# Performance work log

Measured on AMD Instinct MI355X. Metric: run time of the kernel, lower is better.

## Reference

```python
import jax, jax.numpy as jnp
import numpy as np

EPS = 1e-5
DIL = 1
PAD = 1
STRIDE = 1

def conv2d(x, w, stride=1, pad=1, dil=1):
    return jax.lax.conv_general_dilated(x, w, (stride, stride), [(pad, pad), (pad, pad)],
                                        rhs_dilation=(dil, dil),
                                        dimension_numbers=('NCHW', 'OIHW', 'NCHW'))

def batchnorm(x, g, b, m, v):
    inv = g / jnp.sqrt(v + EPS)
    return x * inv[None, :, None, None] + (b - m * inv)[None, :, None, None]

def _bilinear(img, y, x):
    # img: [C,H,W]; y,x: [Ho,Wo] float sample coords; zero padding outside.
    H, W = img.shape[1], img.shape[2]
    y0 = jnp.floor(y); x0 = jnp.floor(x)
    ty = y - y0; tx = x - x0
    y0i = y0.astype(jnp.int32); x0i = x0.astype(jnp.int32)
    def g(yi, xi):
        valid = (yi >= 0) & (yi < H) & (xi >= 0) & (xi < W)
        v = img[:, jnp.clip(yi, 0, H - 1), jnp.clip(xi, 0, W - 1)]  # [C,Ho,Wo]
        return jnp.where(valid[None], v, jnp.zeros((), img.dtype))
    return (g(y0i, x0i) * ((1 - ty) * (1 - tx))[None]
            + g(y0i, x0i + 1) * ((1 - ty) * tx)[None]
            + g(y0i + 1, x0i) * (ty * (1 - tx))[None]
            + g(y0i + 1, x0i + 1) * (ty * tx)[None])

def deform_conv(x, w, offset, stride=1, pad=1, dil=1):
    # offset: [B, 18, Ho, Wo], channels 0:9 = dy per kernel tap (row-major), 9:18 = dx.
    B, C, H, W = x.shape
    Co = w.shape[0]
    Ho = (H + 2 * pad - dil * 2 - 1) // stride + 1
    Wo = (W + 2 * pad - dil * 2 - 1) // stride + 1
    off = offset.reshape(B, 2, 9, Ho, Wo)
    iy = (jnp.arange(Ho) * stride - pad).astype(x.dtype)
    ix = (jnp.arange(Wo) * stride - pad).astype(x.dtype)
    wk = w.reshape(Co, C, 9)
    out = jnp.zeros((B, Co, Ho, Wo), x.dtype)
    for k in range(9):  # fixed 3x3 kernel taps
        ky, kx = k // 3, k % 3
        ys = iy[:, None] + ky * dil + off[:, 0, k]  # [B,Ho,Wo]
        xs = ix[None, :] + kx * dil + off[:, 1, k]
        val = jax.vmap(_bilinear)(x, ys, xs)        # [B,C,Ho,Wo]
        out = out + jnp.einsum('bchw,oc->bohw', val, wk[:, :, k])
    return out

def offset_bias(dil, dtype):
    bw = jnp.array([[-1., 0., 1.]] * 3, dtype) * (dil - 1)
    bh = bw.T
    return jnp.concatenate([bh.reshape(-1), bw.reshape(-1)])  # [18]

def setup_inputs() -> dict:
    key = jax.random.key(0)
    ks = jax.random.split(key, 12)
    B, C, H, W = 8, 256, 56, 56
    inp = {
        'x': jax.random.normal(ks[0], (B, C, H, W), jnp.float32),
        'conv1_w': jax.random.normal(ks[1], (C, C, 3, 3), jnp.float32) * 0.02,
        'bn1_g': jax.random.normal(ks[2], (C,), jnp.float32) * 0.1 + 1.0,
        'bn1_b': jax.random.normal(ks[3], (C,), jnp.float32) * 0.1,
        'bn1_m': jax.random.normal(ks[4], (C,), jnp.float32) * 0.1,
        'bn1_v': jax.random.uniform(ks[5], (C,), jnp.float32) + 0.5,
        'off_w': jax.random.normal(ks[6], (18, C, 3, 3), jnp.float32) * 0.01,
        'off_b': jnp.zeros((18,), jnp.float32),
        'conv2_w': jax.random.normal(ks[7], (C, C, 3, 3), jnp.float32) * 0.02,
        'bn2_g': jax.random.normal(ks[8], (C,), jnp.float32) * 0.1 + 1.0,
        'bn2_b': jax.random.normal(ks[9], (C,), jnp.float32) * 0.1,
        'bn2_m': jax.random.normal(ks[10], (C,), jnp.float32) * 0.1,
        'bn2_v': jax.random.uniform(ks[11], (C,), jnp.float32) + 0.5,
    }
    return inp

def reference(x, conv1_w, bn1_g, bn1_b, bn1_m, bn1_v, off_w, off_b, conv2_w, bn2_g, bn2_b, bn2_m, bn2_v):
    residual = x
    out = conv2d(x, conv1_w, STRIDE, PAD, DIL)
    out = jax.nn.relu(batchnorm(out, bn1_g, bn1_b, bn1_m, bn1_v))
    offset = conv2d(out, off_w, STRIDE, PAD, DIL) + off_b[None, :, None, None]
    offset = offset + offset_bias(DIL, out.dtype)[None, :, None, None]
    out = deform_conv(out, conv2_w, offset, STRIDE, PAD, DIL)
    out = batchnorm(out, bn2_g, bn2_b, bn2_m, bn2_v)
    return jax.nn.relu(out + residual)
```

## Files before the change

kernel.cpp:

```cpp
#include <hip/hip_runtime.h>
#include <hip/hip_fp16.h>

#define NB 8
#define NH 56
#define NW 56
#define NHW 3136
#define NCHW 802816
#define NPIX 25088
#define NHP 58
#define EPSV 1e-5f
#define BUFS 20480
#define TOFN 451584

typedef float f32x4 __attribute__((ext_vector_type(4)));
typedef __bf16 bf16x8 __attribute__((ext_vector_type(8)));
typedef _Float16 f16x8 __attribute__((ext_vector_type(8)));

__device__ __forceinline__ unsigned short f2b(float f) {
  unsigned int u = __float_as_uint(f);
  u += 0x7FFFu + ((u >> 16) & 1u);
  return (unsigned short)(u >> 16);
}
__device__ __forceinline__ unsigned short f2h(float f) {
  return __half_as_ushort(__float2half(f));
}
__device__ __forceinline__ void soft_barrier() {
  __builtin_amdgcn_s_waitcnt(0xC07F);
  __builtin_amdgcn_s_barrier();
}
__device__ __forceinline__ void dma16(const unsigned short* g, unsigned short* l) {
  __builtin_amdgcn_global_load_lds(
      (const __attribute__((address_space(1))) unsigned int*)g,
      (__attribute__((address_space(3))) unsigned int*)l,
      16, 0, 0);
}
__device__ __forceinline__ unsigned int bil2(
    unsigned int c00, unsigned int c01, unsigned int c10, unsigned int c11,
    __half2 W00, __half2 W01, __half2 W10, __half2 W11) {
  __half2 v = __hmul2(W00, *(__half2*)&c00);
  v = __hfma2(W01, *(__half2*)&c01, v);
  v = __hfma2(W10, *(__half2*)&c10, v);
  v = __hfma2(W11, *(__half2*)&c11, v);
  return *(unsigned int*)&v;
}

__global__ __launch_bounds__(256) void clear_borders(
    unsigned short* __restrict__ xbp, unsigned short* __restrict__ t1b,
    float* __restrict__ tof)
{
  int i = blockIdx.x*256 + threadIdx.x;
  int q = i & 31; int pid = i >> 5;
  int b = pid / 228, j = pid % 228;
  int y, x;
  if (j < 58)       { y = 0;  x = j; }
  else if (j < 116) { y = 57; x = j - 58; }
  else { int jj = j - 116; y = 1 + (jj >> 1); x = (jj & 1) * 57; }
  size_t addr = ((size_t)(b*NHP + y)*NHP + x)*256 + q*8;
  uint4 z = make_uint4(0u,0u,0u,0u);
  *(uint4*)(xbp + addr) = z;
  *(uint4*)(t1b + addr) = z;
  int zi = i*8;
  if (zi < TOFN) {
    *(float4*)(tof + zi)     = make_float4(0.f,0.f,0.f,0.f);
    *(float4*)(tof + zi + 4) = make_float4(0.f,0.f,0.f,0.f);
  }
}

__global__ __launch_bounds__(256) void prep_x(
    const float* __restrict__ x, unsigned short* __restrict__ xbp)
{
  __shared__ float T[64][65];
  const int pxt  = blockIdx.x * 64;
  const int cg   = blockIdx.y * 64;
  const int b    = pxt / NHW;
  const int rem0 = pxt % NHW;
  const int t    = threadIdx.x;
  const int pl   = t & 63;
  const int c0   = t >> 6;
  const float* src = x + (size_t)b*NCHW + rem0;
  #pragma unroll
  for (int it = 0; it < 16; ++it) {
    int c = c0 + it*4;
    T[c][pl] = src[(size_t)(cg + c)*NHW + pl];
  }
  __syncthreads();
  const int pr = t >> 5;
  const int cp = t & 31;
  #pragma unroll
  for (int it = 0; it < 8; ++it) {
    int pxl = pr + it*8;
    int rem = rem0 + pxl;
    int ho = rem / NW, wo = rem % NW;
    unsigned int pk = ((unsigned int)f2b(T[cp*2+1][pxl]) << 16) | (unsigned int)f2b(T[cp*2][pxl]);
    *(unsigned int*)(xbp + ((size_t)(b*NHP + ho + 1)*NHP + (wo + 1))*256 + cg + cp*2) = pk;
  }
}

__global__ __launch_bounds__(256) void prep_w_all(
    const float* __restrict__ w1, const float* __restrict__ w2,
    const float* __restrict__ ow,
    unsigned short* __restrict__ w1p, unsigned short* __restrict__ w2p,
    unsigned short* __restrict__ w3p)
{
  int i = blockIdx.x*256 + threadIdx.x;
  if (i < 589824) {
    int co = i / 2304, r = i % 2304, k = r >> 8, ci = r & 255;
    w1p[i] = f2b(w1[((size_t)co*256 + ci)*9 + k]);
  } else if (i < 1179648) {
    int j = i - 589824;
    int co = j / 2304, r = j % 2304, k = r >> 8, ci = r & 255;
    w2p[j] = f2h(w2[((size_t)co*256 + ci)*9 + k]);
  } else {
    int j = i - 1179648;
    int co = j / 2304, r = j % 2304, k = r >> 8, ci = r & 255;
    w3p[j] = (co < 18) ? f2h(ow[((size_t)co*256 + ci)*9 + k]) : (unsigned short)0;
  }
}

__global__ __launch_bounds__(512, 4) void gemm_conv1(
    const unsigned short* __restrict__ xbp, const unsigned short* __restrict__ w1p,
    const float* __restrict__ gam, const float* __restrict__ bet,
    const float* __restrict__ mu,  const float* __restrict__ var,
    unsigned short* __restrict__ t1b)
{
  __shared__ unsigned short SMEM[2*BUFS];

  const int bx   = blockIdx.x;
  const int nbx  = (bx & 7)*49 + (bx >> 3);
  const int m0   = nbx * 64;
  const int t    = threadIdx.x;
  const int lane = t & 63;
  const int wv   = t >> 6;
  const int wvM  = wv & 1;
  const int wvN  = wv >> 1;
  const int quad = lane >> 4;
  const int l15  = lane & 15;

  const int srow = t >> 3;
  const int seg  = t & 7;
  const int swz8 = ((seg ^ (srow & 7))*8);
  const int px  = m0 + srow;
  const int b   = px / NHW, rem = px % NHW;
  const int ho  = rem / NW, wo = rem % NW;
  const unsigned int pbaseA = ((unsigned int)(b*NHP + ho)*NHP + wo)*256u + (unsigned int)swz8;
  const int rowB0 = wv*32 + (lane >> 3);
  const unsigned int bswz = (unsigned int)(((lane & 7) ^ (lane >> 3))*8);
  const int chA = wv*512;

  f32x4 acc[2][4];
  #pragma unroll
  for (int i = 0; i < 2; ++i)
    #pragma unroll
    for (int j = 0; j < 4; ++j) acc[i][j] = (f32x4)(0.f);

  {
    dma16(xbp + pbaseA, &SMEM[chA]);
    #pragma unroll
    for (int j = 0; j < 4; ++j)
      dma16(w1p + (size_t)(rowB0 + j*8)*2304 + bswz, &SMEM[4096 + (wv*4 + j)*512]);
    __syncthreads();
  }

  for (int r = 0; r < 36; ++r) {
    unsigned short* Ac = SMEM + (r & 1)*BUFS;
    unsigned short* Bc = Ac + 4096;
    unsigned short* An = SMEM + ((r + 1) & 1)*BUFS;
    unsigned short* Bn = An + 4096;
    {
      const int rn = (r < 35) ? r + 1 : 35;
      const int kn = rn >> 2, cicn = rn & 3;
      const int kyn = kn/3, kxn = kn - kyn*3;
      const unsigned int koff = (unsigned int)((kyn*NHP + kxn)*256 + cicn*64);
      dma16(xbp + pbaseA + koff, &An[chA]);
      const unsigned int rb = (unsigned int)(rn*64);
      #pragma unroll
      for (int j = 0; j < 4; ++j)
        dma16(w1p + (size_t)(rowB0 + j*8)*2304 + rb + bswz, &Bn[(wv*4 + j)*512]);
    }
    #pragma unroll
    for (int kk = 0; kk < 2; ++kk) {
      const int s8 = (kk*4 + quad) ^ (l15 & 7);
      bf16x8 af[2], bfr[4];
      #pragma unroll
      for (int mt = 0; mt < 2; ++mt)
        af[mt] = *(const bf16x8*)(&Ac[(wvM*32 + mt*16 + l15)*64 + s8*8]);
      #pragma unroll
      for (int nt = 0; nt < 4; ++nt)
        bfr[nt] = *(const bf16x8*)(&Bc[(wvN*64 + nt*16 + l15)*64 + s8*8]);
      #pragma unroll
      for (int mt = 0; mt < 2; ++mt)
        #pragma unroll
        for (int nt = 0; nt < 4; ++nt)
          acc[mt][nt] = __builtin_amdgcn_mfma_f32_16x16x32_bf16(af[mt], bfr[nt], acc[mt][nt], 0, 0, 0);
    }
    __syncthreads();
  }

  unsigned short* Sw = SMEM + wv*2304;
  #pragma unroll
  for (int nt = 0; nt < 4; ++nt) {
    const int co = wvN*64 + nt*16 + l15;
    const float inv  = gam[co] * rsqrtf(var[co] + EPSV);
    const float beta = bet[co] - mu[co]*inv;
    #pragma unroll
    for (int mt = 0; mt < 2; ++mt) {
      #pragma unroll
      for (int rr = 0; rr < 4; ++rr) {
        const int pxl = mt*16 + quad*4 + rr;
        float val = acc[mt][nt][rr]*inv + beta;
        val = val > 0.f ? val : 0.f;
        Sw[pxl*72 + nt*16 + l15] = f2h(val);
      }
    }
  }
  #pragma unroll
  for (int i = 0; i < 4; ++i) {
    const int pxl = (lane >> 3) + 8*i;
    const int sc  = lane & 7;
    uint4 q = *(const uint4*)(&Sw[pxl*72 + sc*8]);
    const int pg = m0 + wvM*32 + pxl;
    const int bb = pg / NHW, rm = pg % NHW;
    const int hh = rm / NW, ww = rm % NW;
    *(uint4*)(t1b + ((size_t)(bb*NHP + hh + 1)*NHP + ww + 1)*256 + wvN*64 + sc*8) = q;
  }
}

__global__ __launch_bounds__(256, 8) void gemm_off(
    const unsigned short* __restrict__ t1b, const unsigned short* __restrict__ w3p,
    const float* __restrict__ ob, float* __restrict__ toff)
{
  __shared__ unsigned short Al[4096];
  __shared__ unsigned short Bl[2048];

  const int bx  = blockIdx.x;
  const int nbx = (bx & 7)*49 + (bx >> 3);
  const int m0  = nbx * 64;
  const int kc = blockIdx.y;
  const int t    = threadIdx.x;
  const int lane = t & 63;
  const int wv   = t >> 6;
  const int quad = lane >> 4;
  const int l15  = lane & 15;

  const int arow = t >> 2;
  const int as4  = t & 3;
  const int axor = arow & 7;
  const int pxa  = m0 + arow;
  const int ba   = pxa / NHW, rema = pxa % NHW;
  const unsigned int pbase = ((unsigned int)(ba*NHP + rema/NW)*NHP + rema%NW)*256u;

  const int brow = t >> 3;
  const int bs   = t & 7;

  f32x4 acc[2];
  #pragma unroll
  for (int nt = 0; nt < 2; ++nt) {
    float init = 0.f;
    if (kc == 0) { int co = nt*16 + l15; init = (co < 18) ? ob[co] : 0.f; }
    acc[nt] = (f32x4)(init);
  }

  uint4 pA0, pA1, pB;
  {
    const int r = kc*9, k = r >> 2, cic = r & 3;
    const int ky = k/3, kx = k - ky*3;
    const unsigned int base = pbase + (unsigned int)((ky*NHP + kx)*256 + cic*64);
    pA0 = *(const uint4*)(t1b + base + as4*8);
    pA1 = *(const uint4*)(t1b + base + (as4+4)*8);
    pB  = *(const uint4*)(w3p + (size_t)brow*2304 + r*64 + bs*8);
  }

  for (int rr = 0; rr < 9; ++rr) {
    const int r = kc*9 + rr;
    __syncthreads();
    *(uint4*)(&Al[arow*64 + ((as4     ^ axor)*8)]) = pA0;
    *(uint4*)(&Al[arow*64 + (((as4+4) ^ axor)*8)]) = pA1;
    *(uint4*)(&Bl[brow*64 + ((bs ^ (brow & 7))*8)]) = pB;
    {
      const int rn = (rr < 8) ? r + 1 : r;
      const int kn = rn >> 2, cicn = rn & 3;
      const int kyn = kn/3, kxn = kn - kyn*3;
      const unsigned int base = pbase + (unsigned int)((kyn*NHP + kxn)*256 + cicn*64);
      pA0 = *(const uint4*)(t1b + base + as4*8);
      pA1 = *(const uint4*)(t1b + base + (as4+4)*8);
      pB  = *(const uint4*)(w3p + (size_t)brow*2304 + rn*64 + bs*8);
    }
    soft_barrier();
    #pragma unroll
    for (int kk = 0; kk < 2; ++kk) {
      const int s8 = (kk*4 + quad) ^ (l15 & 7);
      f16x8 af = *(const f16x8*)(&Al[(wv*16 + l15)*64 + s8*8]);
      #pragma unroll
      for (int nt = 0; nt < 2; ++nt) {
        f16x8 bfr = *(const f16x8*)(&Bl[(nt*16 + l15)*64 + s8*8]);
        acc[nt] = __builtin_amdgcn_mfma_f32_16x16x32_f16(af, bfr, acc[nt], 0, 0, 0);
      }
    }
  }
  #pragma unroll
  for (int nt = 0; nt < 2; ++nt) {
    const int co = nt*16 + l15;
    if (co < 18) {
      #pragma unroll
      for (int rr2 = 0; rr2 < 4; ++rr2) {
        const int pg = m0 + wv*16 + quad*4 + rr2;
        const int bb = pg / NHW, rm = pg % NHW;
        atomicAdd(&toff[(size_t)bb*(18*NHW) + (size_t)co*NHW + rm], acc[nt][rr2]);
      }
    }
  }
}

__global__ __launch_bounds__(512, 4) void gemm_deform(
    const unsigned short* __restrict__ t1b, const unsigned short* __restrict__ w2p,
    const float* __restrict__ toff, const float* __restrict__ xres,
    const float* __restrict__ gam, const float* __restrict__ bet,
    const float* __restrict__ mu,  const float* __restrict__ var,
    float* __restrict__ outp)
{
  __shared__ unsigned short SMEM[2*BUFS];

  const int bid  = blockIdx.x;
  const int nb   = (bid & 7)*49 + (bid >> 3);
  const int m0   = nb * 64;
  const int t    = threadIdx.x;
  const int lane = t & 63;
  const int wv   = t >> 6;
  const int wvM  = wv & 1;
  const int wvN  = wv >> 1;
  const int quad = lane >> 4;
  const int l15  = lane & 15;

  const int srow = t >> 3;
  const int seg  = t & 7;
  const int sxor = srow & 7;
  const int px   = m0 + srow;
  const int b    = px / NHW, rem = px % NHW;
  const int ho   = rem / NW, wo = rem % NW;
  const int obb  = b*(18*NHW) + rem;
  const unsigned int prowb = (unsigned int)(b*NHP);

  const int rowB0 = wv*32 + (lane >> 3);
  const unsigned int bswz = (unsigned int)(((lane & 7) ^ (lane >> 3))*8);

  f32x4 acc[2][4];
  #pragma unroll
  for (int i = 0; i < 2; ++i)
    #pragma unroll
    for (int j = 0; j < 4; ++j) acc[i][j] = (f32x4)(0.f);

  unsigned int o00, o01, o10, o11;
  __half2 W00, W01, W10, W11;
#define COORDS(KK) {                                                   \
    const int ky_ = (KK)/3, kx_ = (KK) - ky_*3;                        \
    const float offy = toff[obb + (KK)*NHW];                           \
    const float offx = toff[obb + (9+(KK))*NHW];                       \
    const float yf = (float)(ho - 1 + ky_) + offy;                     \
    const float xf = (float)(wo - 1 + kx_) + offx;                     \
    const float y0f = floorf(yf), x0f = floorf(xf);                    \
    const float ty = yf - y0f,   tx = xf - x0f;                        \
    const int y0p = (int)y0f + 1, x0p = (int)x0f + 1;                  \
    const int cy0 = min(max(y0p,   0), NHP-1);                         \
    const int cy1 = min(max(y0p+1, 0), NHP-1);                         \
    const int cx0 = min(max(x0p,   0), NHP-1);                         \
    const int cx1 = min(max(x0p+1, 0), NHP-1);                         \
    W00 = __float2half2_rn((1.f-ty)*(1.f-tx));                         \
    W01 = __float2half2_rn((1.f-ty)*tx);                               \
    W10 = __float2half2_rn(ty*(1.f-tx));                               \
    W11 = __float2half2_rn(ty*tx);                                     \
    o00 = ((prowb + cy0)*NHP + cx0)*256u + seg*8u;                     \
    o01 = ((prowb + cy0)*NHP + cx1)*256u + seg*8u;                     \
    o10 = ((prowb + cy1)*NHP + cx0)*256u + seg*8u;                     \
    o11 = ((prowb + cy1)*NHP + cx1)*256u + seg*8u;                     \
  }

#define PACKW(DST) {                                                            \
    uint4 res;                                                                  \
    res.x = bil2(pc00.x, pc01.x, pc10.x, pc11.x, W00, W01, W10, W11);           \
    res.y = bil2(pc00.y, pc01.y, pc10.y, pc11.y, W00, W01, W10, W11);           \
    res.z = bil2(pc00.z, pc01.z, pc10.z, pc11.z, W00, W01, W10, W11);           \
    res.w = bil2(pc00.w, pc01.w, pc10.w, pc11.w, W00, W01, W10, W11);           \
    *(uint4*)(&(DST)[srow*64 + ((seg ^ sxor)*8)]) = res;                        \
  }

#define ISSUEC(RN) {                                                           \
    const unsigned int cio_ = (unsigned int)(((RN) & 3)*64);                   \
    pc00 = *(const uint4*)(t1b + o00 + cio_);                                  \
    pc01 = *(const uint4*)(t1b + o01 + cio_);                                  \
    pc10 = *(const uint4*)(t1b + o10 + cio_);                                  \
    pc11 = *(const uint4*)(t1b + o11 + cio_);                                  \
  }

  uint4 pc00, pc01, pc10, pc11;

  COORDS(0);
  {
    ISSUEC(0);
    #pragma unroll
    for (int j = 0; j < 4; ++j)
      dma16(w2p + (size_t)(rowB0 + j*8)*2304 + bswz, &SMEM[4096 + (wv*4 + j)*512]);
    PACKW(SMEM);
    ISSUEC(1);
    __syncthreads();
  }

  for (int r = 0; r < 36; ++r) {
    unsigned short* Ac = SMEM + (r & 1)*BUFS;
    unsigned short* Bc = Ac + 4096;
    unsigned short* An = SMEM + ((r + 1) & 1)*BUFS;
    unsigned short* Bn = An + 4096;
    PACKW(An);
    {
      const int rnB = (r < 35) ? r + 1 : 35;
      const unsigned int rb = (unsigned int)(rnB*64);
      #pragma unroll
      for (int j = 0; j < 4; ++j)
        dma16(w2p + (size_t)(rowB0 + j*8)*2304 + rb + bswz, &Bn[(wv*4 + j)*512]);
    }
    if ((r & 3) == 2 && r < 34) COORDS((r + 2) >> 2);
    {
      const int rn = (r < 34) ? r + 2 : 35;
      ISSUEC(rn);
    }
    #pragma unroll
    for (int kk = 0; kk < 2; ++kk) {
      const int s8 = (kk*4 + quad) ^ (l15 & 7);
      f16x8 af[2], bfr[4];
      #pragma unroll
      for (int mt = 0; mt < 2; ++mt)
        af[mt] = *(const f16x8*)(&Ac[(wvM*32 + mt*16 + l15)*64 + s8*8]);
      #pragma unroll
      for (int nt = 0; nt < 4; ++nt)
        bfr[nt] = *(const f16x8*)(&Bc[(wvN*64 + nt*16 + l15)*64 + s8*8]);
      #pragma unroll
      for (int mt = 0; mt < 2; ++mt)
        #pragma unroll
        for (int nt = 0; nt < 4; ++nt)
          acc[mt][nt] = __builtin_amdgcn_mfma_f32_16x16x32_f16(af[mt], bfr[nt], acc[mt][nt], 0, 0, 0);
    }
    __syncthreads();
  }
#undef ISSUEC
#undef PACKW
#undef COORDS

  float* Sl = (float*)SMEM + wv*1056;
  const int pxl_r = lane & 31;
  const int csel  = lane >> 5;
  const int pg    = m0 + wvM*32 + pxl_r;
  const int bo    = pg / NHW, remo = pg % NHW;
  const size_t obase = (size_t)bo*NCHW + remo;
  #pragma unroll
  for (int h = 0; h < 2; ++h) {
    #pragma unroll
    for (int nt2 = 0; nt2 < 2; ++nt2) {
      const int nt = h*2 + nt2;
      #pragma unroll
      for (int mt = 0; mt < 2; ++mt) {
        #pragma unroll
        for (int rr = 0; rr < 4; ++rr) {
          const int pxl = mt*16 + quad*4 + rr;
          Sl[pxl*33 + nt2*16 + l15] = acc[mt][nt][rr];
        }
      }
    }
    #pragma unroll
    for (int j = 0; j < 16; ++j) {
      const int col = csel*16 + j;
      const int co  = wvN*64 + h*32 + col;
      const float inv  = gam[co] * rsqrtf(var[co] + EPSV);
      const float beta = bet[co] - mu[co]*inv;
      const size_t off = obase + (size_t)co*NHW;
      float val = Sl[pxl_r*33 + col];
      float o = val*inv + beta + xres[off];
      outp[off] = o > 0.f ? o : 0.f;
    }
  }
}

extern "C" void kernel_launch(void* const* d_in, const int* in_sizes, int n_in,
                              void* d_out, int out_size, void* d_ws, size_t ws_size,
                              hipStream_t stream) {
  const float* x   = (const float*)d_in[0];
  const float* w1  = (const float*)d_in[1];
  const float* g1  = (const float*)d_in[2];
  const float* b1  = (const float*)d_in[3];
  const float* m1  = (const float*)d_in[4];
  const float* v1  = (const float*)d_in[5];
  const float* ow  = (const float*)d_in[6];
  const float* ob  = (const float*)d_in[7];
  const float* w2  = (const float*)d_in[8];
  const float* g2  = (const float*)d_in[9];
  const float* b2  = (const float*)d_in[10];
  const float* m2  = (const float*)d_in[11];
  const float* v2  = (const float*)d_in[12];
  float* out = (float*)d_out;

  const size_t PADSZ = (size_t)NB*NHP*NHP*256;
  unsigned short* xbp = (unsigned short*)d_ws;
  unsigned short* t1b = xbp + PADSZ;
  float*          tof = (float*)(t1b + PADSZ);
  unsigned short* w1p = (unsigned short*)(tof + (size_t)NB*18*NHW);
  unsigned short* w2p = w1p + (size_t)589824;
  unsigned short* w3p = w2p + (size_t)589824;

  clear_borders<<<228, 256, 0, stream>>>(xbp, t1b, tof);
  dim3 gp(392, 4, 1);
  prep_x<<<gp, 256, 0, stream>>>(x, xbp);
  prep_w_all<<<4896, 256, 0, stream>>>(w1, w2, ow, w1p, w2p, w3p);

  gemm_conv1<<<392, 512, 0, stream>>>(xbp, w1p, g1, b1, m1, v1, t1b);
  dim3 go(392, 4, 1);
  gemm_off<<<go, 256, 0, stream>>>(t1b, w3p, ob, tof);
  gemm_deform<<<392, 512, 0, stream>>>(t1b, w2p, tof, x, g2, b2, m2, v2, out);
}
```

Baseline: 228.5 us.

## Halve block size to four waves, each computing a full 64x64 tile

Both big GEMM kernels (conv1 and deform) drop from 8 waves of 512 threads to 4 waves of 256, and each wave now owns all 64 pixel rows times 64 output channels (4x4 MFMA tiles instead of 2x4). This raises per-wave register reuse of the B fragments and halves the number of waves that issue LDS reads for the same A tile. Each thread now issues twice as many DMA copies and, in the deform kernel, computes bilinear samples for 16 channels instead of 8. The cost is more accumulator registers per thread and fewer waves available to hide memory latency.

```diff
diff --git a/kernel.cpp b/kernel.cpp
--- a/kernel.cpp
+++ b/kernel.cpp
@@ -117,7 +117,7 @@
   }
 }
 
-__global__ __launch_bounds__(512, 4) void gemm_conv1(
+__global__ __launch_bounds__(256, 2) void gemm_conv1(
     const unsigned short* __restrict__ xbp, const unsigned short* __restrict__ w1p,
     const float* __restrict__ gam, const float* __restrict__ bet,
     const float* __restrict__ mu,  const float* __restrict__ var,
@@ -131,33 +131,37 @@
   const int t    = threadIdx.x;
   const int lane = t & 63;
   const int wv   = t >> 6;
-  const int wvM  = wv & 1;
-  const int wvN  = wv >> 1;
   const int quad = lane >> 4;
   const int l15  = lane & 15;
 
-  const int srow = t >> 3;
-  const int seg  = t & 7;
-  const int swz8 = ((seg ^ (srow & 7))*8);
-  const int px  = m0 + srow;
-  const int b   = px / NHW, rem = px % NHW;
-  const int ho  = rem / NW, wo = rem % NW;
-  const unsigned int pbaseA = ((unsigned int)(b*NHP + ho)*NHP + wo)*256u + (unsigned int)swz8;
-  const int rowB0 = wv*32 + (lane >> 3);
-  const unsigned int bswz = (unsigned int)(((lane & 7) ^ (lane >> 3))*8);
-  const int chA = wv*512;
-
-  f32x4 acc[2][4];
-  #pragma unroll
-  for (int i = 0; i < 2; ++i)
+  const int lrow = lane >> 3;
+  const int lseg = lane & 7;
+  const int r0 = wv*16 + lrow;
+  const int r1 = r0 + 8;
+  unsigned int pbA0, pbA1;
+  {
+    int p0 = m0 + r0, b0 = p0 / NHW, rm0 = p0 % NHW;
+    pbA0 = ((unsigned int)(b0*NHP + rm0/NW)*NHP + rm0%NW)*256u
+         + (unsigned int)((lseg ^ (r0 & 7))*8);
+    int p1 = m0 + r1, b1 = p1 / NHW, rm1 = p1 % NHW;
+    pbA1 = ((unsigned int)(b1*NHP + rm1/NW)*NHP + rm1%NW)*256u
+         + (unsigned int)((lseg ^ (r1 & 7))*8);
+  }
+  const int rowB0 = wv*64 + lrow;
+  const unsigned int bswz = (unsigned int)((lseg ^ lrow)*8);
+
+  f32x4 acc[4][4];
+  #pragma unroll
+  for (int i = 0; i < 4; ++i)
     #pragma unroll
     for (int j = 0; j < 4; ++j) acc[i][j] = (f32x4)(0.f);
 
   {
-    dma16(xbp + pbaseA, &SMEM[chA]);
-    #pragma unroll
-    for (int j = 0; j < 4; ++j)
-      dma16(w1p + (size_t)(rowB0 + j*8)*2304 + bswz, &SMEM[4096 + (wv*4 + j)*512]);
+    dma16(xbp + pbA0, &SMEM[(wv*2    )*512]);
+    dma16(xbp + pbA1, &SMEM[(wv*2 + 1)*512]);
+    #pragma unroll
+    for (int j = 0; j < 8; ++j)
+      dma16(w1p + (size_t)(rowB0 + j*8)*2304 + bswz, &SMEM[4096 + (wv*8 + j)*512]);
     __syncthreads();
   }
 
@@ -171,24 +175,25 @@
       const int kn = rn >> 2, cicn = rn & 3;
       const int kyn = kn/3, kxn = kn - kyn*3;
       const unsigned int koff = (unsigned int)((kyn*NHP + kxn)*256 + cicn*64);
-      dma16(xbp + pbaseA + koff, &An[chA]);
+      dma16(xbp + pbA0 + koff, &An[(wv*2    )*512]);
+      dma16(xbp + pbA1 + koff, &An[(wv*2 + 1)*512]);
       const unsigned int rb = (unsigned int)(rn*64);
       #pragma unroll
-      for (int j = 0; j < 4; ++j)
-        dma16(w1p + (size_t)(rowB0 + j*8)*2304 + rb + bswz, &Bn[(wv*4 + j)*512]);
+      for (int j = 0; j < 8; ++j)
+        dma16(w1p + (size_t)(rowB0 + j*8)*2304 + rb + bswz, &Bn[(wv*8 + j)*512]);
     }
     #pragma unroll
     for (int kk = 0; kk < 2; ++kk) {
       const int s8 = (kk*4 + quad) ^ (l15 & 7);
-      bf16x8 af[2], bfr[4];
-      #pragma unroll
-      for (int mt = 0; mt < 2; ++mt)
-        af[mt] = *(const bf16x8*)(&Ac[(wvM*32 + mt*16 + l15)*64 + s8*8]);
+      bf16x8 af[4], bfr[4];
+      #pragma unroll
+      for (int mt = 0; mt < 4; ++mt)
+        af[mt] = *(const bf16x8*)(&Ac[(mt*16 + l15)*64 + s8*8]);
       #pragma unroll
       for (int nt = 0; nt < 4; ++nt)
-        bfr[nt] = *(const bf16x8*)(&Bc[(wvN*64 + nt*16 + l15)*64 + s8*8]);
-      #pragma unroll
-      for (int mt = 0; mt < 2; ++mt)
+        bfr[nt] = *(const bf16x8*)(&Bc[(wv*64 + nt*16 + l15)*64 + s8*8]);
+      #pragma unroll
+      for (int mt = 0; mt < 4; ++mt)
         #pragma unroll
         for (int nt = 0; nt < 4; ++nt)
           acc[mt][nt] = __builtin_amdgcn_mfma_f32_16x16x32_bf16(af[mt], bfr[nt], acc[mt][nt], 0, 0, 0);
@@ -196,14 +201,14 @@
     __syncthreads();
   }
 
-  unsigned short* Sw = SMEM + wv*2304;
+  unsigned short* Sw = SMEM + wv*4608;
   #pragma unroll
   for (int nt = 0; nt < 4; ++nt) {
-    const int co = wvN*64 + nt*16 + l15;
+    const int co = wv*64 + nt*16 + l15;
     const float inv  = gam[co] * rsqrtf(var[co] + EPSV);
     const float beta = bet[co] - mu[co]*inv;
     #pragma unroll
-    for (int mt = 0; mt < 2; ++mt) {
+    for (int mt = 0; mt < 4; ++mt) {
       #pragma unroll
       for (int rr = 0; rr < 4; ++rr) {
         const int pxl = mt*16 + quad*4 + rr;
@@ -214,14 +219,14 @@
     }
   }
   #pragma unroll
-  for (int i = 0; i < 4; ++i) {
+  for (int i = 0; i < 8; ++i) {
     const int pxl = (lane >> 3) + 8*i;
     const int sc  = lane & 7;
     uint4 q = *(const uint4*)(&Sw[pxl*72 + sc*8]);
-    const int pg = m0 + wvM*32 + pxl;
+    const int pg = m0 + pxl;
     const int bb = pg / NHW, rm = pg % NHW;
     const int hh = rm / NW, ww = rm % NW;
-    *(uint4*)(t1b + ((size_t)(bb*NHP + hh + 1)*NHP + ww + 1)*256 + wvN*64 + sc*8) = q;
+    *(uint4*)(t1b + ((size_t)(bb*NHP + hh + 1)*NHP + ww + 1)*256 + wv*64 + sc*8) = q;
   }
 }
 
@@ -311,7 +316,7 @@
   }
 }
 
-__global__ __launch_bounds__(512, 4) void gemm_deform(
+__global__ __launch_bounds__(256, 2) void gemm_deform(
     const unsigned short* __restrict__ t1b, const unsigned short* __restrict__ w2p,
     const float* __restrict__ toff, const float* __restrict__ xres,
     const float* __restrict__ gam, const float* __restrict__ bet,
@@ -326,13 +331,11 @@
   const int t    = threadIdx.x;
   const int lane = t & 63;
   const int wv   = t >> 6;
-  const int wvM  = wv & 1;
-  const int wvN  = wv >> 1;
   const int quad = lane >> 4;
   const int l15  = lane & 15;
 
-  const int srow = t >> 3;
-  const int seg  = t & 7;
+  const int srow = t >> 2;
+  const int s2   = (t & 3)*2;
   const int sxor = srow & 7;
   const int px   = m0 + srow;
   const int b    = px / NHW, rem = px % NHW;
@@ -340,12 +343,14 @@
   const int obb  = b*(18*NHW) + rem;
   const unsigned int prowb = (unsigned int)(b*NHP);
 
-  const int rowB0 = wv*32 + (lane >> 3);
-  const unsigned int bswz = (unsigned int)(((lane & 7) ^ (lane >> 3))*8);
-
-  f32x4 acc[2][4];
-  #pragma unroll
-  for (int i = 0; i < 2; ++i)
+  const int lrow = lane >> 3;
+  const int lseg = lane & 7;
+  const int rowB0 = wv*64 + lrow;
+  const unsigned int bswz = (unsigned int)((lseg ^ lrow)*8);
+
+  f32x4 acc[4][4];
+  #pragma unroll
+  for (int i = 0; i < 4; ++i)
     #pragma unroll
     for (int j = 0; j < 4; ++j) acc[i][j] = (f32x4)(0.f);
 
@@ -368,37 +373,46 @@
     W01 = __float2half2_rn((1.f-ty)*tx);                               \
     W10 = __float2half2_rn(ty*(1.f-tx));                               \
     W11 = __float2half2_rn(ty*tx);                                     \
-    o00 = ((prowb + cy0)*NHP + cx0)*256u + seg*8u;                     \
-    o01 = ((prowb + cy0)*NHP + cx1)*256u + seg*8u;                     \
-    o10 = ((prowb + cy1)*NHP + cx0)*256u + seg*8u;                     \
-    o11 = ((prowb + cy1)*NHP + cx1)*256u + seg*8u;                     \
+    o00 = ((prowb + cy0)*NHP + cx0)*256u + s2*8u;                      \
+    o01 = ((prowb + cy0)*NHP + cx1)*256u + s2*8u;                      \
+    o10 = ((prowb + cy1)*NHP + cx0)*256u + s2*8u;                      \
+    o11 = ((prowb + cy1)*NHP + cx1)*256u + s2*8u;                      \
   }
 
 #define PACKW(DST) {                                                            \
-    uint4 res;                                                                  \
-    res.x = bil2(pc00.x, pc01.x, pc10.x, pc11.x, W00, W01, W10, W11);           \
-    res.y = bil2(pc00.y, pc01.y, pc10.y, pc11.y, W00, W01, W10, W11);           \
-    res.z = bil2(pc00.z, pc01.z, pc10.z, pc11.z, W00, W01, W10, W11);           \
-    res.w = bil2(pc00.w, pc01.w, pc10.w, pc11.w, W00, W01, W10, W11);           \
-    *(uint4*)(&(DST)[srow*64 + ((seg ^ sxor)*8)]) = res;                        \
+    uint4 ra, rb2;                                                              \
+    ra.x  = bil2(c00a.x, c01a.x, c10a.x, c11a.x, W00, W01, W10, W11);           \
+    ra.y  = bil2(c00a.y, c01a.y, c10a.y, c11a.y, W00, W01, W10, W11);           \
+    ra.z  = bil2(c00a.z, c01a.z, c10a.z, c11a.z, W00, W01, W10, W11);           \
+    ra.w  = bil2(c00a.w, c01a.w, c10a.w, c11a.w, W00, W01, W10, W11);           \
+    rb2.x = bil2(c00b.x, c01b.x, c10b.x, c11b.x, W00, W01, W10, W11);           \
+    rb2.y = bil2(c00b.y, c01b.y, c10b.y, c11b.y, W00, W01, W10, W11);           \
+    rb2.z = bil2(c00b.z, c01b.z, c10b.z, c11b.z, W00, W01, W10, W11);           \
+    rb2.w = bil2(c00b.w, c01b.w, c10b.w, c11b.w, W00, W01, W10, W11);           \
+    *(uint4*)(&(DST)[srow*64 + ((s2     ^ sxor)*8)]) = ra;                      \
+    *(uint4*)(&(DST)[srow*64 + (((s2+1) ^ sxor)*8)]) = rb2;                     \
   }
 
 #define ISSUEC(RN) {                                                           \
     const unsigned int cio_ = (unsigned int)(((RN) & 3)*64);                   \
-    pc00 = *(const uint4*)(t1b + o00 + cio_);                                  \
-    pc01 = *(const uint4*)(t1b + o01 + cio_);                                  \
-    pc10 = *(const uint4*)(t1b + o10 + cio_);                                  \
-    pc11 = *(const uint4*)(t1b + o11 + cio_);                                  \
-  }
-
-  uint4 pc00, pc01, pc10, pc11;
+    c00a = *(const uint4*)(t1b + o00 + cio_);                                  \
+    c00b = *(const uint4*)(t1b + o00 + cio_ + 8);                              \
+    c01a = *(const uint4*)(t1b + o01 + cio_);                                  \
+    c01b = *(const uint4*)(t1b + o01 + cio_ + 8);                              \
+    c10a = *(const uint4*)(t1b + o10 + cio_);                                  \
+    c10b = *(const uint4*)(t1b + o10 + cio_ + 8);                              \
+    c11a = *(const uint4*)(t1b + o11 + cio_);                                  \
+    c11b = *(const uint4*)(t1b + o11 + cio_ + 8);                              \
+  }
+
+  uint4 c00a, c00b, c01a, c01b, c10a, c10b, c11a, c11b;
 
   COORDS(0);
   {
     ISSUEC(0);
     #pragma unroll
-    for (int j = 0; j < 4; ++j)
-      dma16(w2p + (size_t)(rowB0 + j*8)*2304 + bswz, &SMEM[4096 + (wv*4 + j)*512]);
+    for (int j = 0; j < 8; ++j)
+      dma16(w2p + (size_t)(rowB0 + j*8)*2304 + bswz, &SMEM[4096 + (wv*8 + j)*512]);
     PACKW(SMEM);
     ISSUEC(1);
     __syncthreads();
@@ -414,8 +428,8 @@
       const int rnB = (r < 35) ? r + 1 : 35;
       const unsigned int rb = (unsigned int)(rnB*64);
       #pragma unroll
-      for (int j = 0; j < 4; ++j)
-        dma16(w2p + (size_t)(rowB0 + j*8)*2304 + rb + bswz, &Bn[(wv*4 + j)*512]);
+      for (int j = 0; j < 8; ++j)
+        dma16(w2p + (size_t)(rowB0 + j*8)*2304 + rb + bswz, &Bn[(wv*8 + j)*512]);
     }
     if ((r & 3) == 2 && r < 34) COORDS((r + 2) >> 2);
     {
@@ -425,15 +439,15 @@
     #pragma unroll
     for (int kk = 0; kk < 2; ++kk) {
       const int s8 = (kk*4 + quad) ^ (l15 & 7);
-      f16x8 af[2], bfr[4];
-      #pragma unroll
-      for (int mt = 0; mt < 2; ++mt)
-        af[mt] = *(const f16x8*)(&Ac[(wvM*32 + mt*16 + l15)*64 + s8*8]);
+      f16x8 af[4], bfr[4];
+      #pragma unroll
+      for (int mt = 0; mt < 4; ++mt)
+        af[mt] = *(const f16x8*)(&Ac[(mt*16 + l15)*64 + s8*8]);
       #pragma unroll
       for (int nt = 0; nt < 4; ++nt)
-        bfr[nt] = *(const f16x8*)(&Bc[(wvN*64 + nt*16 + l15)*64 + s8*8]);
-      #pragma unroll
-      for (int mt = 0; mt < 2; ++mt)
+        bfr[nt] = *(const f16x8*)(&Bc[(wv*64 + nt*16 + l15)*64 + s8*8]);
+      #pragma unroll
+      for (int mt = 0; mt < 4; ++mt)
         #pragma unroll
         for (int nt = 0; nt < 4; ++nt)
           acc[mt][nt] = __builtin_amdgcn_mfma_f32_16x16x32_f16(af[mt], bfr[nt], acc[mt][nt], 0, 0, 0);
@@ -447,33 +461,36 @@
   float* Sl = (float*)SMEM + wv*1056;
   const int pxl_r = lane & 31;
   const int csel  = lane >> 5;
-  const int pg    = m0 + wvM*32 + pxl_r;
-  const int bo    = pg / NHW, remo = pg % NHW;
-  const size_t obase = (size_t)bo*NCHW + remo;
-  #pragma unroll
-  for (int h = 0; h < 2; ++h) {
-    #pragma unroll
-    for (int nt2 = 0; nt2 < 2; ++nt2) {
-      const int nt = h*2 + nt2;
-      #pragma unroll
-      for (int mt = 0; mt < 2; ++mt) {
+  #pragma unroll
+  for (int mh = 0; mh < 2; ++mh) {
+    const int pg    = m0 + mh*32 + pxl_r;
+    const int bo    = pg / NHW, remo = pg % NHW;
+    const size_t obase = (size_t)bo*NCHW + remo;
+    #pragma unroll
+    for (int h = 0; h < 2; ++h) {
+      #pragma unroll
+      for (int nt2 = 0; nt2 < 2; ++nt2) {
+        const int nt = h*2 + nt2;
         #pragma unroll
-        for (int rr = 0; rr < 4; ++rr) {
-          const int pxl = mt*16 + quad*4 + rr;
-          Sl[pxl*33 + nt2*16 + l15] = acc[mt][nt][rr];
+        for (int mt2 = 0; mt2 < 2; ++mt2) {
+          #pragma unroll
+          for (int rr = 0; rr < 4; ++rr) {
+            const int pxl = mt2*16 + quad*4 + rr;
+            Sl[pxl*33 + nt2*16 + l15] = acc[mh*2 + mt2][nt][rr];
+          }
         }
       }
-    }
-    #pragma unroll
-    for (int j = 0; j < 16; ++j) {
-      const int col = csel*16 + j;
-      const int co  = wvN*64 + h*32 + col;
-      const float inv  = gam[co] * rsqrtf(var[co] + EPSV);
-      const float beta = bet[co] - mu[co]*inv;
-      const size_t off = obase + (size_t)co*NHW;
-      float val = Sl[pxl_r*33 + col];
-      float o = val*inv + beta + xres[off];
-      outp[off] = o > 0.f ? o : 0.f;
+      #pragma unroll
+      for (int j = 0; j < 16; ++j) {
+        const int col = csel*16 + j;
+        const int co  = wv*64 + h*32 + col;
+        const float inv  = gam[co] * rsqrtf(var[co] + EPSV);
+        const float beta = bet[co] - mu[co]*inv;
+        const size_t off = obase + (size_t)co*NHW;
+        float val = Sl[pxl_r*33 + col];
+        float o = val*inv + beta + xres[off];
+        outp[off] = o > 0.f ? o : 0.f;
+      }
     }
   }
 }
@@ -509,8 +526,8 @@
   prep_x<<<gp, 256, 0, stream>>>(x, xbp);
   prep_w_all<<<4896, 256, 0, stream>>>(w1, w2, ow, w1p, w2p, w3p);
 
-  gemm_conv1<<<392, 512, 0, stream>>>(xbp, w1p, g1, b1, m1, v1, t1b);
+  gemm_conv1<<<392, 256, 0, stream>>>(xbp, w1p, g1, b1, m1, v1, t1b);
   dim3 go(392, 4, 1);
   gemm_off<<<go, 256, 0, stream>>>(t1b, w3p, ob, tof);
-  gemm_deform<<<392, 512, 0, stream>>>(t1b, w2p, tof, x, g2, b2, m2, v2, out);
-}
+  gemm_deform<<<392, 256, 0, stream>>>(t1b, w2p, tof, x, g2, b2, m2, v2, out);
+}
```

Result: slower. 236.6 us (+3.5%).
